# Kernel optimization log

Hardware: AMD Instinct MI355X
Metric: run time of the kernel (lower is better)

Reference implementation:

```python
import jax, jax.numpy as jnp
import numpy as np
from jax import lax


def setup_inputs() -> dict:
    key = jax.random.key(0)
    k1, k2 = jax.random.split(key)
    B, Cin, T, H, W_ = 4, 16, 31, 128, 128
    Chid = 16
    inputs = jax.random.normal(k1, (B, Cin, T, H, W_), dtype=jnp.float32)
    # Conv3d(Cin, 2*Chid, kernel=3, padding=1) weights, OIDHW layout
    W = jax.random.normal(k2, (2 * Chid, Cin, 3, 3, 3), dtype=jnp.float32) * 0.05
    b = jnp.zeros((2 * Chid,), dtype=jnp.float32)
    return {"inputs": inputs, "W": W, "b": b}


def _fo_pool(Z, F):
    # Z, F: [B, C, T, H, W]; recurrence h_t = f_t * h_{t-1} + (1 - f_t) * z_t, h_{-1} = 0
    Zt = jnp.moveaxis(Z, 2, 0)  # [T, B, C, H, W]
    Ft = jnp.moveaxis(F, 2, 0)

    def step(h, zf):
        z, f = zf
        h = f * h + (1.0 - f) * z
        return h, h

    h0 = jnp.zeros_like(Zt[0])
    _, hs = lax.scan(step, h0, (Zt, Ft))
    return jnp.moveaxis(hs, 0, 2)  # back to [B, C, T, H, W]


def reference(inputs, W, b):
    # gated conv: Conv3d with SAME padding (kernel 3, padding 1)
    gates = lax.conv_general_dilated(
        inputs, W, window_strides=(1, 1, 1), padding="SAME",
        dimension_numbers=("NCDHW", "OIDHW", "NCDHW"))
    gates = gates + b[None, :, None, None, None]
    Chid = W.shape[0] // 2
    Z = jnp.tanh(gates[:, :Chid])
    F = jax.nn.sigmoid(gates[:, Chid:])
    return _fo_pool(Z, F)
```

## Files before the change

### kernel.cpp

```cpp
#include <hip/hip_runtime.h>
#include <cstdint>
#include <cstddef>

#define CIN     16
#define CHID    16
#define T_DIM   31
#define HW_     16384
#define CH_STRIDE 507904
#define TILE_H  4
#define TILE_W  32
#define SH      6
#define SW      34
#define SPOS    (SH * SW)
#define PSTR    24
#define SLICE_SH (SPOS * PSTR)

typedef short bf16x8 __attribute__((ext_vector_type(8)));
typedef float f32x16 __attribute__((ext_vector_type(16)));

__device__ __forceinline__ unsigned bf16_bits(float x) {
  unsigned u = __builtin_bit_cast(unsigned, x);
  u += 0x7FFFu + ((u >> 16) & 1u);
  return u >> 16;
}
__device__ __forceinline__ unsigned cvt_pk_bf16(float lo, float hi) {
  unsigned r;
  asm("v_cvt_pk_bf16_f32 %0, %1, %2" : "=v"(r) : "v"(lo), "v"(hi));
  return r;
}

__global__ __launch_bounds__(256, 2)
void qrnn3d_v11(const float* __restrict__ in, const float* __restrict__ Wg,
                const float* __restrict__ bg, float* __restrict__ out) {
  __shared__ __align__(16) short xs[4][SLICE_SH];

  const int tid = threadIdx.x;
  const int bid = blockIdx.x;
  const int lin  = ((bid & 7) << 6) | (bid >> 3);
  const int b    = lin >> 7;
  const int tile = lin & 127;
  const int h0   = (tile >> 2) * TILE_H;
  const int w0   = (tile & 3) * TILE_W;

  const int lane = tid & 63;
  const int wid  = tid >> 6;
  const int col  = lane & 31;
  const int half = lane >> 5;

  bf16x8 wfrag[27];
#pragma unroll
  for (int tau = 0; tau < 27; ++tau) {
    bf16x8 f;
#pragma unroll
    for (int j = 0; j < 8; ++j)
      f[j] = (short)bf16_bits(Wg[col * 432 + (half * 8 + j) * 27 + tau]);
    wfrag[tau] = f;
  }

  f32x16 accInit;
  int voff[8];
#pragma unroll
  for (int r = 0; r < 8; ++r) {
    int oc = (r & 3) + 8 * (r >> 2) + 4 * half;
    accInit[r]     = bg[oc];
    accInit[r + 8] = bg[oc + 16];
    voff[r] = (b * CHID + oc) * CH_STRIDE + (h0 + wid) * 128 + (w0 + col);
  }

  const float* gp[4];
  int  lso[4];
  bool stv[4], ldv[4];
#pragma unroll
  for (int i = 0; i < 4; ++i) {
    int p   = tid + i * 256;
    int q   = p & 15;
    int c4  = (p >> 4) & 3;
    int j   = p >> 6;
    int pos = j * 16 + q;
    stv[i]  = (pos < SPOS);
    int hh  = pos / SW;
    int ww  = pos - hh * SW;
    int gh  = h0 + hh - 1, gw = w0 + ww - 1;
    ldv[i]  = stv[i] && ((unsigned)gh < 128u) && ((unsigned)gw < 128u);
    int sp  = ldv[i] ? (gh * 128 + gw) : 0;
    gp[i]   = in + (size_t)(b * CIN + c4 * 4) * CH_STRIDE + sp;
    lso[i]  = pos * PSTR + c4 * 4;
  }

#define LOADV(tz, vv)                                                \
  do {                                                               \
    if ((tz) <= 30) {                                                \
      const int toff = (tz) * HW_;                                   \
      _Pragma("unroll")                                              \
      for (int i = 0; i < 4; ++i) {                                  \
        _Pragma("unroll")                                            \
        for (int k = 0; k < 4; ++k)                                  \
          vv[i][k] = ldv[i] ? gp[i][toff + k * CH_STRIDE] : 0.0f;    \
      }                                                              \
    } else {                                                         \
      _Pragma("unroll")                                              \
      for (int i = 0; i < 4; ++i) {                                  \
        _Pragma("unroll")                                            \
        for (int k = 0; k < 4; ++k) vv[i][k] = 0.0f;                 \
      }                                                              \
    }                                                                \
  } while (0)

#define STOREV(vv, slot)                                             \
  do {                                                               \
    short* dst = &xs[(slot)][0];                                     \
    _Pragma("unroll")                                                \
    for (int i = 0; i < 4; ++i) {                                    \
      if (stv[i]) {                                                  \
        uint2 u;                                                     \
        u.x = cvt_pk_bf16(vv[i][0], vv[i][1]);                       \
        u.y = cvt_pk_bf16(vv[i][2], vv[i][3]);                       \
        *reinterpret_cast<uint2*>(dst + lso[i]) = u;                 \
      }                                                              \
    }                                                                \
  } while (0)

  int lb[9];
#pragma unroll
  for (int kh = 0; kh < 3; ++kh)
#pragma unroll
    for (int kw = 0; kw < 3; ++kw)
      lb[kh * 3 + kw] = ((wid + kh) * SW + (col + kw)) * PSTR + half * 8;

  float hst[8];
#pragma unroll
  for (int r = 0; r < 8; ++r) hst[r] = 0.0f;

  const float C_TANH = 2.8853900817779268f;
  const float C_SIG  = 1.4426950408889634f;

  auto compute = [&](int t) {
    const short* base = &xs[0][0];
    const short* sA = base + ((t + 3) & 3) * SLICE_SH;
    const short* sB = base + ((t    ) & 3) * SLICE_SH;
    const short* sC = base + ((t + 1) & 3) * SLICE_SH;

    f32x16 acc0 = accInit;
    f32x16 acc1;
#pragma unroll
    for (int i = 0; i < 16; ++i) acc1[i] = 0.0f;

#pragma unroll
    for (int kd = 0; kd < 3; ++kd) {
      const short* sp = (kd == 0) ? sA : (kd == 1) ? sB : sC;
#pragma unroll
      for (int u = 0; u < 9; ++u) {
        const int tau = kd * 9 + u;
        bf16x8 xb = *reinterpret_cast<const bf16x8*>(sp + lb[u]);
        if (tau & 1)
          acc1 = __builtin_amdgcn_mfma_f32_32x32x16_bf16(wfrag[tau], xb, acc1, 0, 0, 0);
        else
          acc0 = __builtin_amdgcn_mfma_f32_32x32x16_bf16(wfrag[tau], xb, acc0, 0, 0, 0);
      }
    }

    float* outT = out + (size_t)t * HW_;
#pragma unroll
    for (int r = 0; r < 8; ++r) {
      float zg = acc0[r] + acc1[r];
      float fg = acc0[r + 8] + acc1[r + 8];
      float ez = exp2f(zg * C_TANH);
      float z  = __builtin_fmaf(-2.0f, __builtin_amdgcn_rcpf(ez + 1.0f), 1.0f);
      float ef = exp2f(-fg * C_SIG);
      float f  = __builtin_amdgcn_rcpf(1.0f + ef);
      float h  = __builtin_fmaf(f, hst[r] - z, z);
      hst[r]   = h;
      outT[voff[r]] = h;
    }
  };

  float vA[4][4], vB[4][4];
  LOADV(0, vA); STOREV(vA, 0);
  LOADV(1, vA); STOREV(vA, 1);
  LOADV(2, vA);
  for (int i = tid; i < SLICE_SH / 2; i += 256)
    reinterpret_cast<unsigned*>(&xs[3][0])[i] = 0u;
  __syncthreads();

#pragma unroll 1
  for (int t = 0; t < 30; t += 2) {
    LOADV(t + 3, vB);
    STOREV(vA, (t + 2) & 3);
    compute(t);
    __syncthreads();
    LOADV(t + 4, vA);
    STOREV(vB, (t + 3) & 3);
    compute(t + 1);
    __syncthreads();
  }
  compute(30);

#undef LOADV
#undef STOREV
}

extern "C" void kernel_launch(void* const* d_in, const int* in_sizes, int n_in,
                              void* d_out, int out_size, void* d_ws, size_t ws_size,
                              hipStream_t stream) {
  const float* in = (const float*)d_in[0];
  const float* Wg = (const float*)d_in[1];
  const float* bg = (const float*)d_in[2];
  float* out      = (float*)d_out;
  (void)in_sizes; (void)n_in; (void)out_size; (void)d_ws; (void)ws_size;
  qrnn3d_v11<<<dim3(512), dim3(256), 0, stream>>>(in, Wg, bg, out);
}
```

Before: 123.2 us.

## Reuse each input slice across three rotating temporal accumulators

Restructures the time loop so each loaded input slice is read from shared memory once and fed to three rotating accumulators, one per temporal kernel tap (kd). This replaces re-reading three slices per step. Shared memory drops from four slice buffers to three, and one barrier per step replaces the double-buffered schedule. The cost is more live accumulator registers (three f32x16) plus nine staged fragments, which may pressure the two-blocks-per-CU occupancy target. Each step also now puts a barrier directly before its MFMAs, which reduces load/compute overlap.

```diff
diff --git a/kernel.cpp b/kernel.cpp
--- a/kernel.cpp
+++ b/kernel.cpp
@@ -29,10 +29,12 @@
   return r;
 }
 
+#define MFMA(W, X, C) __builtin_amdgcn_mfma_f32_32x32x16_bf16((W), (X), (C), 0, 0, 0)
+
 __global__ __launch_bounds__(256, 2)
-void qrnn3d_v11(const float* __restrict__ in, const float* __restrict__ Wg,
+void qrnn3d_v13(const float* __restrict__ in, const float* __restrict__ Wg,
                 const float* __restrict__ bg, float* __restrict__ out) {
-  __shared__ __align__(16) short xs[4][SLICE_SH];
+  __shared__ __align__(16) short xs[3][SLICE_SH];
 
   const int tid = threadIdx.x;
   const int bid = blockIdx.x;
@@ -127,6 +129,8 @@
     for (int kw = 0; kw < 3; ++kw)
       lb[kh * 3 + kw] = ((wid + kh) * SW + (col + kw)) * PSTR + half * 8;
 
+#define RD(SLOT, U) (*(const bf16x8*)(&xs[(SLOT)][0] + lb[(U)]))
+
   float hst[8];
 #pragma unroll
   for (int r = 0; r < 8; ++r) hst[r] = 0.0f;
@@ -134,69 +138,75 @@
   const float C_TANH = 2.8853900817779268f;
   const float C_SIG  = 1.4426950408889634f;
 
-  auto compute = [&](int t) {
-    const short* base = &xs[0][0];
-    const short* sA = base + ((t + 3) & 3) * SLICE_SH;
-    const short* sB = base + ((t    ) & 3) * SLICE_SH;
-    const short* sC = base + ((t + 1) & 3) * SLICE_SH;
-
-    f32x16 acc0 = accInit;
-    f32x16 acc1;
-#pragma unroll
-    for (int i = 0; i < 16; ++i) acc1[i] = 0.0f;
-
-#pragma unroll
-    for (int kd = 0; kd < 3; ++kd) {
-      const short* sp = (kd == 0) ? sA : (kd == 1) ? sB : sC;
-#pragma unroll
-      for (int u = 0; u < 9; ++u) {
-        const int tau = kd * 9 + u;
-        bf16x8 xb = *reinterpret_cast<const bf16x8*>(sp + lb[u]);
-        if (tau & 1)
-          acc1 = __builtin_amdgcn_mfma_f32_32x32x16_bf16(wfrag[tau], xb, acc1, 0, 0, 0);
-        else
-          acc0 = __builtin_amdgcn_mfma_f32_32x32x16_bf16(wfrag[tau], xb, acc0, 0, 0, 0);
-      }
-    }
-
-    float* outT = out + (size_t)t * HW_;
-#pragma unroll
-    for (int r = 0; r < 8; ++r) {
-      float zg = acc0[r] + acc1[r];
-      float fg = acc0[r + 8] + acc1[r + 8];
-      float ez = exp2f(zg * C_TANH);
-      float z  = __builtin_fmaf(-2.0f, __builtin_amdgcn_rcpf(ez + 1.0f), 1.0f);
-      float ef = exp2f(-fg * C_SIG);
-      float f  = __builtin_amdgcn_rcpf(1.0f + ef);
-      float h  = __builtin_fmaf(f, hst[r] - z, z);
-      hst[r]   = h;
-      outT[voff[r]] = h;
-    }
-  };
-
+#define EPI(T, ACC)                                                  \
+  do {                                                               \
+    float* outT_ = out + (size_t)(T) * HW_;                          \
+    _Pragma("unroll")                                                \
+    for (int r_ = 0; r_ < 8; ++r_) {                                 \
+      float zg_ = (ACC)[r_], fg_ = (ACC)[r_ + 8];                    \
+      float ez_ = exp2f(zg_ * C_TANH);                               \
+      float z_  = __builtin_fmaf(-2.0f, __builtin_amdgcn_rcpf(ez_ + 1.0f), 1.0f); \
+      float ef_ = exp2f(-fg_ * C_SIG);                               \
+      float f_  = __builtin_amdgcn_rcpf(1.0f + ef_);                 \
+      float h_  = __builtin_fmaf(f_, hst[r_] - z_, z_);              \
+      hst[r_]   = h_;                                                \
+      outT_[voff[r_]] = h_;                                          \
+    }                                                                \
+  } while (0)
+
+#define STEP(T, SRD, SWR, AC, AM, AN, VCUR, VNXT)                    \
+  do {                                                               \
+    LOADV((T) + 3, VNXT);                                            \
+    STOREV(VCUR, SWR);                                               \
+    __syncthreads();                                                 \
+    bf16x8 xb_[9];                                                   \
+    _Pragma("unroll")                                                \
+    for (int u_ = 0; u_ < 9; ++u_) xb_[u_] = RD(SRD, u_);            \
+    AN = MFMA(wfrag[0], xb_[0], accInit);                            \
+    _Pragma("unroll")                                                \
+    for (int u_ = 1; u_ < 9; ++u_) AN = MFMA(wfrag[u_], xb_[u_], AN);\
+    _Pragma("unroll")                                                \
+    for (int u_ = 0; u_ < 9; ++u_) AM = MFMA(wfrag[9 + u_], xb_[u_], AM); \
+    _Pragma("unroll")                                                \
+    for (int u_ = 0; u_ < 9; ++u_) AC = MFMA(wfrag[18 + u_], xb_[u_], AC); \
+    EPI(T, AC);                                                      \
+  } while (0)
+
+  f32x16 A0, A1, A2;
   float vA[4][4], vB[4][4];
+
   LOADV(0, vA); STOREV(vA, 0);
-  LOADV(1, vA); STOREV(vA, 1);
+  LOADV(1, vB); STOREV(vB, 1);
   LOADV(2, vA);
-  for (int i = tid; i < SLICE_SH / 2; i += 256)
-    reinterpret_cast<unsigned*>(&xs[3][0])[i] = 0u;
   __syncthreads();
+  {
+    bf16x8 xb_[9];
+#pragma unroll
+    for (int u = 0; u < 9; ++u) xb_[u] = RD(0, u);
+    A0 = MFMA(wfrag[9], xb_[0], accInit);
+#pragma unroll
+    for (int u = 1; u < 9; ++u) A0 = MFMA(wfrag[9 + u], xb_[u], A0);
+    A1 = MFMA(wfrag[0], xb_[0], accInit);
+#pragma unroll
+    for (int u = 1; u < 9; ++u) A1 = MFMA(wfrag[u], xb_[u], A1);
+  }
 
 #pragma unroll 1
-  for (int t = 0; t < 30; t += 2) {
-    LOADV(t + 3, vB);
-    STOREV(vA, (t + 2) & 3);
-    compute(t);
-    __syncthreads();
-    LOADV(t + 4, vA);
-    STOREV(vB, (t + 3) & 3);
-    compute(t + 1);
-    __syncthreads();
-  }
-  compute(30);
+  for (int tb = 0; tb < 30; tb += 6) {
+    STEP(tb + 0, 1, 2, A0, A1, A2, vA, vB);
+    STEP(tb + 1, 2, 0, A1, A2, A0, vB, vA);
+    STEP(tb + 2, 0, 1, A2, A0, A1, vA, vB);
+    STEP(tb + 3, 1, 2, A0, A1, A2, vB, vA);
+    STEP(tb + 4, 2, 0, A1, A2, A0, vA, vB);
+    STEP(tb + 5, 0, 1, A2, A0, A1, vB, vA);
+  }
+  EPI(30, A0);
 
 #undef LOADV
 #undef STOREV
+#undef RD
+#undef EPI
+#undef STEP
 }
 
 extern "C" void kernel_launch(void* const* d_in, const int* in_sizes, int n_in,
@@ -207,5 +217,5 @@
   const float* bg = (const float*)d_in[2];
   float* out      = (float*)d_out;
   (void)in_sizes; (void)n_in; (void)out_size; (void)d_ws; (void)ws_size;
-  qrnn3d_v11<<<dim3(512), dim3(256), 0, stream>>>(in, Wg, bg, out);
-}
+  qrnn3d_v13<<<dim3(512), dim3(256), 0, stream>>>(in, Wg, bg, out);
+}
```

Measured after the change: 227.9 us. 84.9% more time.
